# Performance work log

Hardware: AMD Instinct MI355X
Metric: run time of the kernel (lower is better)

Reference implementation:

```python
import math
import jax, jax.numpy as jnp
import numpy as np

VOCAB = 32000
D = 512
H = 4
N_LAYER = 4
B = 4
S = 512


def _ln(z, g, eps=1e-5):
    m = jnp.mean(z, axis=-1, keepdims=True)
    v = jnp.var(z, axis=-1, keepdims=True)
    return (z - m) * jax.lax.rsqrt(v + eps) * g


def setup_inputs() -> dict:
    key = jax.random.key(0)
    ks = jax.random.split(key, 6)
    std = 0.02
    x = jax.random.randint(ks[0], (B, S), 0, VOCAB)
    wte = jax.random.normal(ks[1], (VOCAB, D), jnp.float32) * std
    wpe = jax.random.normal(ks[2], (S + 1, D), jnp.float32) * std
    W_q = jax.random.normal(ks[3], (H, D, D), jnp.float32) * std
    W_k = jax.random.normal(ks[4], (H, D, D), jnp.float32) * std
    W_o = jax.random.normal(ks[5], (D, H * D), jnp.float32) * (std / math.sqrt(2 * N_LAYER))
    return {
        "x": x, "wte": wte, "wpe": wpe,
        "g_e": jnp.ones((D,), jnp.float32),
        "g_p": jnp.ones((D,), jnp.float32),
        "g_f": jnp.ones((D,), jnp.float32),
        "W_q": W_q, "W_k": W_k, "W_o": W_o,
    }


def reference(x, wte, wpe, g_e, g_p, g_f, W_q, W_k, W_o):
    b, s = x.shape
    d = wte.shape[1]

    # token / position embeddings (dropout p=0 -> identity)
    e = _ln(wte[x], g_e)                      # (B,S,D)
    p = _ln(wpe[: s + 1], g_p)                # (S+1,D), identical across batch
    x_i, x_j = p[:-1], p[1:]                  # keys / queries

    # custom QK attention kernel (batch-independent since p is shared)
    Q = jnp.einsum('sd,hde->hse', x_j, W_q)   # (H,S,D)
    K = jnp.einsum('sd,hde->hse', x_i, W_k)
    krn = jnp.einsum('hse,hte->hst', Q, K) / math.sqrt(d)
    krn = jnp.clip(krn, -10.0, 10.0)
    causal = jnp.tril(jnp.ones((s, s), bool))
    krn = jnp.where(causal, krn, -jnp.inf)
    krn = jax.nn.softmax(krn, axis=-1)        # (H,S,S)

    # W_N: row i scaled by 1/(i+1)
    coef = 1.0 / (1.0 + jnp.arange(s, dtype=e.dtype))  # (S,)

    f_k = jnp.zeros_like(e)
    for _ in range(N_LAYER):
        # soft codebook retrieval against full vocab
        scores = jnp.einsum('vd,bsd->bvs', wte, f_k)     # (B,V,S)
        R = jax.nn.softmax(scores, axis=-1)
        Rsum = jnp.sum(R, axis=1)                        # (B,S)
        ex_wte = jnp.einsum('bvs,vd->bsd', R, wte) / Rsum[..., None]
        Vm = e - ex_wte                                  # (B,S,D)
        delta = jnp.einsum('hst,btd->bhsd', krn, Vm)     # (B,H,S,D)
        delta = delta * coef[None, None, :, None]
        delta = delta.transpose(0, 2, 1, 3).reshape(b, s, -1)  # (B,S,H*D)
        f_k = f_k + delta @ W_o.T

    out = _ln(f_k, g_f)
    logits = out[:, -1:, :] @ wte.T                      # (B,1,V)
    return logits
```

## Files before the change

### kernel.cpp

```cpp
#include <hip/hip_runtime.h>
#include <stdint.h>


typedef __attribute__((ext_vector_type(8))) short s16x8;
typedef __attribute__((ext_vector_type(4))) short s16x4;
typedef __attribute__((ext_vector_type(4))) float f32x4;

__device__ __forceinline__ short f2bf(float f) {
  unsigned u = __float_as_uint(f);
  unsigned r = (u + 0x7FFFu + ((u >> 16) & 1u)) >> 16;
  return (short)r;
}
__device__ __forceinline__ float bf2f(short u) {
  unsigned v = ((unsigned)(unsigned short)u) << 16;
  return __uint_as_float(v);
}
__device__ __forceinline__ unsigned char f2fp8_full(float x) {
  unsigned u = __float_as_uint(x);
  unsigned sg = (u >> 24) & 0x80;
  u &= 0x7fffffff;
  float a = __uint_as_float(u);
  if (a >= 448.f) return (unsigned char)(sg | 0x7e);
  if (a < 0.015625f) {
    int m = (int)rintf(a * 512.f);
    return (unsigned char)(sg | m);
  }
  u += 0x7FFFFu + ((u >> 20) & 1u);
  int eb = (int)((u >> 23) & 0xff) - 120;
  if (eb >= 16) return (unsigned char)(sg | 0x7e);
  return (unsigned char)(sg | (eb << 3) | ((u >> 20) & 7));
}

__device__ __forceinline__ void load16(const void* g, void* l) {
  __builtin_amdgcn_global_load_lds(
      (__attribute__((address_space(1))) void*)g,
      (__attribute__((address_space(3))) void*)l, 16, 0, 0);
}

template <int EPI, int TERMS>
__global__ void __launch_bounds__(256) gemm64(
    const short* __restrict__ Ag, const short* __restrict__ Bg,
    const short* __restrict__ A2g, const short* __restrict__ B2g,
    void* __restrict__ Cg, short* __restrict__ C2g, int lda, int ldb, int ldc,
    int klen, int k0_mul, int zdiv, long sAq, long sAr, long sBq, long sBr,
    long sCq, long sCr) {
  const int tid = threadIdx.x;
  const int z = blockIdx.z;
  const int zq = z / zdiv, zr = z % zdiv;
  const long aOff = zq * sAq + zr * sAr + (long)zr * k0_mul;
  const long bOff = zq * sBq + zr * sBr + (long)zr * k0_mul;
  const long cOff = zq * sCq + zr * sCr;

  __shared__ __align__(16) short As[64 * 64];
  __shared__ __align__(16) short Bs[64 * 64];

  const long m0 = (long)blockIdx.x * 64;
  const long n0 = (long)blockIdx.y * 64;

  const int wave = tid >> 6, lane = tid & 63;
  const int wm = (wave >> 1) * 32, wn = (wave & 1) * 32;
  const int mlan = lane & 15, kg = lane >> 4;

  f32x4 acc[2][2] = {};

  const int g_src = ((lane & 7) ^ (lane >> 3)) * 8;
  const int lrow = lane >> 3;
  short* lA = As + wave * 1024 + lane * 8;
  short* lB = Bs + wave * 1024 + lane * 8;

  const int gi0 = ((kg ^ (mlan & 7)) * 8);
  const int gi1 = gi0 ^ 32;

  const int nk = klen >> 6;
#pragma unroll 1
  for (int t = 0; t < TERMS; ++t) {
    const short* Abase = ((TERMS == 3 && t == 2) ? A2g : Ag) + aOff;
    const short* Bbase = ((TERMS == 3 && t == 1) ? B2g : Bg) + bOff;
    const short* ga = Abase + (m0 + wave * 16 + lrow) * (long)lda + g_src;
    const short* gb = Bbase + (n0 + wave * 16 + lrow) * (long)ldb + g_src;
#pragma unroll 1
    for (int kt = 0; kt < nk; ++kt) {
      const int kb = kt * 64;
      __syncthreads();
      load16(ga + kb, lA);
      load16(ga + 8 * (long)lda + kb, lA + 512);
      load16(gb + kb, lB);
      load16(gb + 8 * (long)ldb + kb, lB + 512);
      __syncthreads();
      s16x8 af[2][2], bq[2][2];
      const short* pA = As + (wm + mlan) * 64;
      const short* pB = Bs + (wn + mlan) * 64;
#pragma unroll
      for (int i = 0; i < 2; ++i) {
        af[0][i] = *(const s16x8*)(pA + i * 1024 + gi0);
        af[1][i] = *(const s16x8*)(pA + i * 1024 + gi1);
        bq[0][i] = *(const s16x8*)(pB + i * 1024 + gi0);
        bq[1][i] = *(const s16x8*)(pB + i * 1024 + gi1);
      }
#pragma unroll
      for (int h = 0; h < 2; ++h)
#pragma unroll
        for (int mi = 0; mi < 2; ++mi)
#pragma unroll
          for (int ni = 0; ni < 2; ++ni)
            acc[mi][ni] = __builtin_amdgcn_mfma_f32_16x16x32_bf16(
                af[h][mi], bq[h][ni], acc[mi][ni], 0, 0, 0);
    }
  }

  const int rq = (lane >> 4) * 4;
#pragma unroll
  for (int mi = 0; mi < 2; ++mi) {
#pragma unroll
    for (int ni = 0; ni < 2; ++ni) {
#pragma unroll
      for (int r = 0; r < 4; ++r) {
        long row = m0 + wm + mi * 16 + rq + r;
        long col = n0 + wn + ni * 16 + mlan;
        float v = acc[mi][ni][r];
        long o = cOff + row * (long)ldc + col;
        if (EPI == 3) {
          ((float*)Cg)[o] = v;
        } else if (EPI == 4) {
          short h = f2bf(v);
          ((short*)Cg)[o] = h;
          C2g[o] = f2bf(v - bf2f(h));
        } else {
          ((short*)Cg)[o] = f2bf(v);
        }
      }
    }
  }
}

__global__ void __launch_bounds__(256) gemm8tri(
    const unsigned char* __restrict__ Ag, short* __restrict__ Cg) {
  const int tid = threadIdx.x;
  const int zr = blockIdx.z;
  const long kOff = (long)zr * 640;
  const long cOff = (long)zr * 262144;

  __shared__ __align__(16) unsigned char As[128 * 128];
  __shared__ __align__(16) unsigned char Bs[128 * 128];

  int t = blockIdx.x;
  int ty = 0;
  while ((ty + 1) * (ty + 2) / 2 <= t) ++ty;
  int tx = t - ty * (ty + 1) / 2;
  const long m0 = (long)tx * 128;
  const long n0 = (long)ty * 128;

  const int wave = tid >> 6, lane = tid & 63;
  const int wm = (wave >> 1) * 64, wn = (wave & 1) * 64;
  const int mlan = lane & 15, kg = lane >> 4;

  f32x4 acc[4][4] = {};

  const int g_src = ((lane & 7) ^ (lane >> 3)) * 16;
  const int lrow = lane >> 3;
  unsigned char* lA = As + wave * 4096 + lane * 16;
  unsigned char* lB = Bs + wave * 4096 + lane * 16;

  const unsigned char* ga = Ag + kOff + (m0 + wave * 32 + lrow) * 32000L + g_src;
  const unsigned char* gb = Ag + kOff + (n0 + wave * 32 + lrow) * 32000L + g_src;

#pragma unroll 1
  for (int kt = 0; kt < 5; ++kt) {
    const int kb = kt * 128;
    __syncthreads();
    load16(ga + kb, lA);
    load16(ga + 8 * 32000L + kb, lA + 1024);
    load16(ga + 16 * 32000L + kb, lA + 2048);
    load16(ga + 24 * 32000L + kb, lA + 3072);
    load16(gb + kb, lB);
    load16(gb + 8 * 32000L + kb, lB + 1024);
    load16(gb + 16 * 32000L + kb, lB + 2048);
    load16(gb + 24 * 32000L + kb, lB + 3072);
    __syncthreads();
    const unsigned char* pA = As + (wm + mlan) * 128;
    const unsigned char* pB = Bs + (wn + mlan) * 128;
#pragma unroll
    for (int h = 0; h < 4; ++h) {
      const int go = (((2 * h + (kg >> 1)) ^ (mlan & 7)) * 16) + (kg & 1) * 8;
      long af[4], bq[4];
#pragma unroll
      for (int i = 0; i < 4; ++i) {
        af[i] = *(const long*)(pA + i * 2048 + go);
        bq[i] = *(const long*)(pB + i * 2048 + go);
      }
#pragma unroll
      for (int mi = 0; mi < 4; ++mi)
#pragma unroll
        for (int ni = 0; ni < 4; ++ni)
          acc[mi][ni] = __builtin_amdgcn_mfma_f32_16x16x32_fp8_fp8(
              af[mi], bq[ni], acc[mi][ni], 0, 0, 0);
    }
  }

  const int rq = (lane >> 4) * 4;
#pragma unroll
  for (int mi = 0; mi < 4; ++mi)
#pragma unroll
    for (int ni = 0; ni < 4; ++ni)
#pragma unroll
      for (int r = 0; r < 4; ++r) {
        long row = m0 + wm + mi * 16 + rq + r;
        long col = n0 + wn + ni * 16 + mlan;
        Cg[cOff + row * 512 + col] = f2bf(acc[mi][ni][r]);
      }
}

__global__ void __launch_bounds__(256) ln_both(
    const int* __restrict__ tok, const float* __restrict__ wte,
    const float* __restrict__ wpe, const float* __restrict__ g_e,
    const float* __restrict__ g_p, float* __restrict__ e32,
    short* __restrict__ p_hi, short* __restrict__ p_lo) {
  int r = blockIdx.x, tid = threadIdx.x;
  bool tokm = r < 2048;
  const float* in =
      tokm ? wte + (long)tok[r] * 512 : wpe + (long)(r - 2048) * 512;
  const float* g = tokm ? g_e : g_p;
  int d = tid * 2;
  float2 v = *(const float2*)(in + d);
  float s1 = v.x + v.y;
  float s2 = v.x * v.x + v.y * v.y;
  __shared__ float red[20];
  for (int o = 32; o > 0; o >>= 1) {
    s1 += __shfl_down(s1, o);
    s2 += __shfl_down(s2, o);
  }
  int wave = tid >> 6, lane = tid & 63;
  if (lane == 0) { red[wave] = s1; red[wave + 8] = s2; }
  __syncthreads();
  if (tid == 0) {
    float a = red[0] + red[1] + red[2] + red[3];
    float b = red[8] + red[9] + red[10] + red[11];
    float mean = a * (1.f / 512.f);
    float var = b * (1.f / 512.f) - mean * mean;
    red[16] = mean;
    red[17] = 1.0f / sqrtf(var + 1e-5f);
  }
  __syncthreads();
  float mean = red[16], rs = red[17];
  float2 gg = *(const float2*)(g + d);
  float y0 = (v.x - mean) * rs * gg.x;
  float y1 = (v.y - mean) * rs * gg.y;
  if (tokm) {
    long o = (long)r * 512 + d;
    e32[o] = y0;
    e32[o + 1] = y1;
  } else {
    long o = (long)(r - 2048) * 512 + d;
    short h0 = f2bf(y0), h1 = f2bf(y1);
    p_hi[o] = h0; p_hi[o + 1] = h1;
    p_lo[o] = f2bf(y0 - bf2f(h0));
    p_lo[o + 1] = f2bf(y1 - bf2f(h1));
  }
}

__global__ void __launch_bounds__(256) softmax_krn_k(
    const float* __restrict__ raw, float* __restrict__ klast,
    short* __restrict__ k16) {
  int bx = blockIdx.x;
  int h = bx >> 9, s = bx & 511;
  long base = ((long)h * 512 + s) * 512;
  int tid = threadIdx.x;
  const float scale = 0.04419417382415922f;
  float e0 = 0.f, e1 = 0.f, l = 0.f;
  int t0 = tid, t1 = tid + 256;
  if (t0 <= s) {
    float v = raw[base + t0] * scale;
    v = fminf(fmaxf(v, -10.f), 10.f);
    e0 = __expf(v); l += e0;
  }
  if (t1 <= s) {
    float v = raw[base + t1] * scale;
    v = fminf(fmaxf(v, -10.f), 10.f);
    e1 = __expf(v); l += e1;
  }
  for (int o = 32; o > 0; o >>= 1) l += __shfl_down(l, o);
  __shared__ float red[10];
  int wave = tid >> 6, lane = tid & 63;
  if (lane == 0) red[wave] = l;
  __syncthreads();
  if (tid == 0) red[8] = 1.0f / (red[0] + red[1] + red[2] + red[3]);
  __syncthreads();
  float inv = red[8];
  float coef = 1.0f / (1.0f + (float)s);
  k16[base + t0] = f2bf(e0 * inv * coef);
  k16[base + t1] = f2bf(e1 * inv * coef);
  if (s == 511) {
    klast[h * 512 + t0] = e0 * inv;
    klast[h * 512 + t1] = e1 * inv;
  }
}

__global__ void __launch_bounds__(256) prep_w(
    const float* __restrict__ Wq, const float* __restrict__ Wk,
    const float* __restrict__ W_o, short* __restrict__ hi,
    short* __restrict__ lo, short* __restrict__ wo16,
    float* __restrict__ WoT) {
  int z = blockIdx.z;
  int tid = threadIdx.x;
  __shared__ float tl[64][65];
  if (z < 8) {
    const float* inp =
        (z < 4) ? Wq + (long)z * 262144 : Wk + (long)(z - 4) * 262144;
    short* ho = hi + (long)z * 262144;
    short* lop = lo + (long)z * 262144;
    int c0 = blockIdx.x * 64, r0 = blockIdx.y * 64;
    for (int it = 0; it < 16; ++it) {
      int idx = it * 256 + tid;
      int rr = idx >> 6, cc = idx & 63;
      tl[rr][cc] = inp[(long)(r0 + rr) * 512 + (c0 + cc)];
    }
    __syncthreads();
    for (int it = 0; it < 16; ++it) {
      int idx = it * 256 + tid;
      int rr = idx >> 6, cc = idx & 63;
      float v = tl[cc][rr];
      long o = (long)(c0 + rr) * 512 + (r0 + cc);
      short hh = f2bf(v);
      ho[o] = hh;
      lop[o] = f2bf(v - bf2f(hh));
    }
  } else {
    int c0 = (blockIdx.x + (z - 8) * 8) * 64, r0 = blockIdx.y * 64;
    for (int it = 0; it < 16; ++it) {
      int idx = it * 256 + tid;
      int rr = idx >> 6, cc = idx & 63;
      long o = (long)(r0 + rr) * 2048 + (c0 + cc);
      float v = W_o[o];
      tl[rr][cc] = v;
      wo16[o] = f2bf(v);
    }
    __syncthreads();
    for (int it = 0; it < 16; ++it) {
      int idx = it * 256 + tid;
      int rr = idx >> 6, cc = idx & 63;
      WoT[(long)(c0 + rr) * 512 + (r0 + cc)] = tl[cc][rr];
    }
  }
}

__global__ void __launch_bounds__(256) prep_wte(
    const float* __restrict__ wte, unsigned char* __restrict__ wT8,
    float* __restrict__ cm) {
  int c0 = blockIdx.x * 64, r0 = blockIdx.y * 64;
  __shared__ float tl[64][65];
  __shared__ float cred[4][64];
  int tid = threadIdx.x, w = tid >> 6, cx = tid & 63;
  float csum = 0.f;
  for (int it = 0; it < 16; ++it) {
    int idx = it * 256 + tid;
    int rr = idx >> 6, cc = idx & 63;
    float v = wte[(long)(r0 + rr) * 512 + c0 + cc];
    tl[rr][cc] = v;
    csum += v;
  }
  cred[w][cx] = csum;
  __syncthreads();
  if (w == 0) {
    float s = cred[0][cx] + cred[1][cx] + cred[2][cx] + cred[3][cx];
    atomicAdd(&cm[c0 + cx], s * (1.f / 32000.f));
  }
  for (int it = 0; it < 16; ++it) {
    int idx = it * 256 + tid;
    int rr = idx >> 6, cc = idx & 63;
    wT8[(long)(c0 + rr) * 32000 + r0 + cc] = f2fp8_full(tl[cc][rr] * 64.f);
  }
}

__global__ void __launch_bounds__(256) gsum_k(
    const short* __restrict__ part, short* __restrict__ G16) {
  int t = blockIdx.x;
  int ty = 0;
  while ((ty + 1) * (ty + 2) / 2 <= t) ++ty;
  int tx = t - ty * (ty + 1) / 2;
  int r0 = blockIdx.y * 16;
  int tid = threadIdx.x;
  float acc[8] = {};
  for (int z = 0; z < 50; ++z) {
    const short* p = part + (long)z * 262144;
#pragma unroll
    for (int it = 0; it < 8; ++it) {
      int idx = it * 256 + tid;
      int r = idx >> 7, c = idx & 127;
      acc[it] += bf2f(p[(long)(tx * 128 + r0 + r) * 512 + ty * 128 + c]);
    }
  }
  __shared__ short tl[16][132];
#pragma unroll
  for (int it = 0; it < 8; ++it) {
    int idx = it * 256 + tid;
    int r = idx >> 7, c = idx & 127;
    short h = f2bf(acc[it] * (1.f / 4096.f));
    G16[(long)(tx * 128 + r0 + r) * 512 + ty * 128 + c] = h;
    tl[r][c] = h;
  }
  if (tx == ty) return;
  __syncthreads();
#pragma unroll
  for (int it = 0; it < 8; ++it) {
    int idx = it * 256 + tid;
    int c = idx >> 4, r = idx & 15;
    G16[(long)(ty * 128 + c) * 512 + tx * 128 + r0 + r] = tl[r][c];
  }
}

__global__ void __launch_bounds__(256) gmean_k(
    const short* __restrict__ gc, const float* __restrict__ rowdot,
    float* __restrict__ fbarG, float* __restrict__ fbcm,
    float* __restrict__ dl) {
  int b = blockIdx.y, e0 = blockIdx.x * 64;
  int tid = threadIdx.x, w = tid >> 6, lane = tid & 63;
  dl[(long)(b * 8 + blockIdx.x) * 256 + tid] = 0.f;
  float acc = 0.f;
  const short* p = gc + (long)b * 262144 + e0 + lane;
  for (int s = w * 128; s < w * 128 + 128; ++s) acc += bf2f(p[(long)s * 512]);
  __shared__ float red[4][64];
  red[w][lane] = acc;
  __syncthreads();
  if (w == 0)
    fbarG[b * 512 + e0 + lane] =
        (red[0][lane] + red[1][lane] + red[2][lane] + red[3][lane]) *
        (1.f / 512.f);
  if (blockIdx.x == 0) {
    float r2 = rowdot[b * 512 + tid] + rowdot[b * 512 + 256 + tid];
    for (int o = 32; o > 0; o >>= 1) r2 += __shfl_down(r2, o);
    __shared__ float rr[4];
    if (lane == 0) rr[w] = r2;
    __syncthreads();
    if (tid == 0) fbcm[b] = (rr[0] + rr[1] + rr[2] + rr[3]) * (1.f / 512.f);
  }
}

__global__ void __launch_bounds__(256) vm_k(
    const float* __restrict__ e32, const short* __restrict__ gc,
    const float* __restrict__ cm, const float* __restrict__ fbarG,
    const float* __restrict__ rowdot, const float* __restrict__ fbcm,
    const float* __restrict__ klast, int useCm, int store,
    short* __restrict__ vmT, float* __restrict__ dl) {
  int b = blockIdx.z, t0 = blockIdx.y * 64, e0 = blockIdx.x * 64;
  __shared__ short tl[64][72];
  __shared__ float kl[4][64];
  __shared__ float ri[64];
  __shared__ float cmv[64];
  __shared__ float fbg[64];
  __shared__ float dred[4][4][64];
  int tid = threadIdx.x;
  int w = tid >> 6, cx = tid & 63;
  kl[w][cx] = klast[w * 512 + t0 + cx];
  if (tid < 64)
    ri[tid] =
        useCm ? 1.f : 1.0f / (1.0f + rowdot[b * 512 + t0 + tid] - fbcm[b]);
  if (tid >= 64 && tid < 128) cmv[tid - 64] = cm[e0 + tid - 64];
  if (tid >= 128 && tid < 192)
    fbg[tid - 128] = useCm ? 0.f : fbarG[b * 512 + e0 + tid - 128];
  __syncthreads();
  long base = ((long)b * 512 + t0) * 512 + e0;
  float accH[4] = {0.f, 0.f, 0.f, 0.f};
  for (int it = 0; it < 16; ++it) {
    int idx = it * 256 + tid;
    int rr = idx >> 6, cc = idx & 63;
    long o = base + (long)rr * 512 + cc;
    float ex;
    if (useCm)
      ex = cmv[cc];
    else
      ex = (cmv[cc] + (bf2f(gc[o]) - fbg[cc]) * (1.f / 32000.f)) * ri[rr];
    float v = e32[o] - ex;
    if (store) tl[rr][cc] = f2bf(v);
#pragma unroll
    for (int h = 0; h < 4; ++h) accH[h] += v * kl[h][rr];
  }
#pragma unroll
  for (int h = 0; h < 4; ++h) dred[w][h][cx] = accH[h];
  __syncthreads();
  if (store) {
    for (int it = 0; it < 16; ++it) {
      int idx = it * 256 + tid;
      int rr = idx >> 6, cc = idx & 63;
      vmT[((long)b * 512 + (e0 + rr)) * 512 + (t0 + cc)] = tl[cc][rr];
    }
  }
  float s = dred[0][w][cx] + dred[1][w][cx] + dred[2][w][cx] + dred[3][w][cx];
  atomicAdd(&dl[(long)b * 2048 + w * 512 + e0 + cx], s * (1.f / 512.f));
}

__global__ void __launch_bounds__(256) flast_k(
    const float* __restrict__ dl, const float* __restrict__ WoT,
    float* __restrict__ fl, float* __restrict__ rowdot) {
  int b = blockIdx.y, d0 = blockIdx.x * 64;
  int tid = threadIdx.x, w = tid >> 6, lane = tid & 63;
  int g = (blockIdx.y * 8 + blockIdx.x) * 256 + tid;
  if (g < 2048) rowdot[g] = 0.f;
  __shared__ float ds[2048];
  __shared__ float red[4][64];
  for (int i = tid; i < 2048; i += 256) ds[i] = dl[(long)b * 2048 + i];
  __syncthreads();
  float acc = 0.f;
  const float* wp = WoT + (long)(w * 512) * 512 + d0 + lane;
  for (int k = 0; k < 512; ++k) acc += ds[w * 512 + k] * wp[(long)k * 512];
  red[w][lane] = acc;
  __syncthreads();
  if (w == 0) {
    float s = red[0][lane] + red[1][lane] + red[2][lane] + red[3][lane];
    fl[(long)b * 512 + d0 + lane] += s;
  }
}

__global__ void __launch_bounds__(256) fkupdate_k(
    const short* __restrict__ part, const float* __restrict__ cm,
    float* __restrict__ fk32, short* __restrict__ fk16,
    float* __restrict__ rowdot) {
  long i = (long)blockIdx.x * 256 + threadIdx.x;
  float4 s = ((const float4*)fk32)[i];
#pragma unroll
  for (int p = 0; p < 4; ++p) {
    s16x4 h = *(const s16x4*)(part + (long)p * 1048576 + i * 4);
    s.x += bf2f(h[0]); s.y += bf2f(h[1]);
    s.z += bf2f(h[2]); s.w += bf2f(h[3]);
  }
  ((float4*)fk32)[i] = s;
  s16x4 o;
  o[0] = f2bf(s.x); o[1] = f2bf(s.y); o[2] = f2bf(s.z); o[3] = f2bf(s.w);
  *(s16x4*)(fk16 + i * 4) = o;
  float4 cmv = ((const float4*)cm)[i & 127];
  float d = s.x * cmv.x + s.y * cmv.y + s.z * cmv.z + s.w * cmv.w;
  for (int off = 32; off > 0; off >>= 1) d += __shfl_down(d, off);
  if ((threadIdx.x & 63) == 0) atomicAdd(&rowdot[i >> 7], d);
}

__global__ void __launch_bounds__(256) logits_k(
    const float* __restrict__ flast, const float* __restrict__ g_f,
    const float* __restrict__ wte, float* __restrict__ out) {
  int tid = threadIdx.x, wave = tid >> 6, lane = tid & 63;
  __shared__ float oln[4][512];
  __shared__ float red[20];
  for (int b = 0; b < 4; ++b) {
    int d = tid * 2;
    float2 v = *(const float2*)(flast + b * 512 + d);
    float s1 = v.x + v.y;
    float s2 = v.x * v.x + v.y * v.y;
    for (int o = 32; o > 0; o >>= 1) {
      s1 += __shfl_down(s1, o);
      s2 += __shfl_down(s2, o);
    }
    if (lane == 0) { red[wave] = s1; red[wave + 8] = s2; }
    __syncthreads();
    if (tid == 0) {
      float a = red[0] + red[1] + red[2] + red[3];
      float bb = red[8] + red[9] + red[10] + red[11];
      float mean = a * (1.f / 512.f);
      float var = bb * (1.f / 512.f) - mean * mean;
      red[16] = mean;
      red[17] = 1.0f / sqrtf(var + 1e-5f);
    }
    __syncthreads();
    float mean = red[16], rs = red[17];
    float2 gg = *(const float2*)(g_f + d);
    oln[b][d] = (v.x - mean) * rs * gg.x;
    oln[b][d + 1] = (v.y - mean) * rs * gg.y;
    __syncthreads();
  }
  float o[4][8];
#pragma unroll
  for (int b = 0; b < 4; b++)
#pragma unroll
    for (int j = 0; j < 8; j++) o[b][j] = oln[b][lane * 8 + j];
  int vbase = blockIdx.x * 64 + wave * 16;
  for (int i = 0; i < 16; i++) {
    int v = vbase + i;
    const float* row = wte + (long)v * 512 + lane * 8;
    float4 x0 = *(const float4*)row;
    float4 x1 = *(const float4*)(row + 4);
    float xr[8] = {x0.x, x0.y, x0.z, x0.w, x1.x, x1.y, x1.z, x1.w};
    float d0 = 0, d1 = 0, d2 = 0, d3 = 0;
#pragma unroll
    for (int j = 0; j < 8; j++) {
      d0 += o[0][j] * xr[j]; d1 += o[1][j] * xr[j];
      d2 += o[2][j] * xr[j]; d3 += o[3][j] * xr[j];
    }
    for (int off = 32; off > 0; off >>= 1) {
      d0 += __shfl_down(d0, off); d1 += __shfl_down(d1, off);
      d2 += __shfl_down(d2, off); d3 += __shfl_down(d3, off);
    }
    if (lane == 0) {
      out[v] = d0; out[32000 + v] = d1; out[64000 + v] = d2;
      out[96000 + v] = d3;
    }
  }
}

extern "C" void kernel_launch(void* const* d_in, const int* in_sizes, int n_in,
                              void* d_out, int out_size, void* d_ws,
                              size_t ws_size, hipStream_t stream) {
  (void)in_sizes; (void)n_in; (void)out_size;
  const int* x = (const int*)d_in[0];
  const float* wte = (const float*)d_in[1];
  const float* wpe = (const float*)d_in[2];
  const float* g_e = (const float*)d_in[3];
  const float* g_p = (const float*)d_in[4];
  const float* g_f = (const float*)d_in[5];
  const float* W_q = (const float*)d_in[6];
  const float* W_k = (const float*)d_in[7];
  const float* W_o = (const float*)d_in[8];
  float* out = (float*)d_out;

  char* ws = (char*)d_ws;
  size_t off = 0;
  auto alloc = [&](size_t b) {
    size_t o = off;
    off += (b + 255) & ~(size_t)255;
    return o;
  };
  const long HS = 262144;
  unsigned char* wT8 = (unsigned char*)(ws + alloc(512L * 32000));
  char* u = ws + alloc(10L * 1048576 * 2);
  short* wqkt_hi = (short*)u;
  short* wqkt_lo = (short*)(u + 4194304);
  short* qk_hi = (short*)(u + 8388608);
  short* qk_lo = (short*)(u + 12582912);
  float* sATT = (float*)(u + 16777216);
  short* fkpart = (short*)u;
  short* wo16 = (short*)(ws + alloc(512L * 2048 * 2));
  float* WoT = (float*)(ws + alloc(2048L * 512 * 4));
  short* p_hi = (short*)(ws + alloc(513L * 512 * 2));
  short* p_lo = (short*)(ws + alloc(513L * 512 * 2));
  float* e32 = (float*)(ws + alloc(2048L * 512 * 4));
  size_t zero_off = off;
  float* colmean = (float*)(ws + alloc(512 * 4));
  float* dl = (float*)(ws + alloc(4L * 2048 * 4));
  float* flast = (float*)(ws + alloc(4L * 512 * 4));
  float* fk32 = (float*)(ws + alloc(2048L * 512 * 4));
  size_t zero_len = off - zero_off;
  float* klast = (float*)(ws + alloc(4L * 512 * 4));
  short* krn16 = (short*)(ws + alloc(4L * HS * 2));
  short* Gpart16 = (short*)(ws + alloc(50L * HS * 2));
  short* G16 = (short*)(ws + alloc(512L * 512 * 2));
  short* fk16b = (short*)(ws + alloc(2048L * 512 * 2));
  short* gc16 = (short*)(ws + alloc(2048L * 512 * 2));
  float* fbarG = (float*)(ws + alloc(4L * 512 * 4));
  float* rowdot = (float*)(ws + alloc(2052L * 4));
  float* fbcm = rowdot + 2048;
  short* vmT16 = (short*)(ws + alloc(2048L * 512 * 2));
  short* delta16 = (short*)(ws + alloc(2048L * 2048 * 2));
  if (off > ws_size) return;

  hipMemsetAsync(ws + zero_off, 0, zero_len, stream);

  prep_wte<<<dim3(8, 500), 256, 0, stream>>>(wte, wT8, colmean);
  gemm8tri<<<dim3(10, 1, 50), 256, 0, stream>>>(wT8, Gpart16);
  gsum_k<<<dim3(10, 8), 256, 0, stream>>>(Gpart16, G16);
  prep_w<<<dim3(8, 8, 12), 256, 0, stream>>>(W_q, W_k, W_o, wqkt_hi, wqkt_lo,
                                             wo16, WoT);
  ln_both<<<2561, 256, 0, stream>>>(x, wte, wpe, g_e, g_p, e32, p_hi, p_lo);

  gemm64<4, 3><<<dim3(8, 8, 8), 256, 0, stream>>>(
      p_hi + 512, wqkt_hi, p_lo + 512, wqkt_lo, qk_hi, qk_lo, 512, 512, 512,
      512, 0, 4,  -512,  0,  4 * HS,  HS,
       4 * HS,  HS);
  gemm64<3, 3><<<dim3(8, 8, 4), 256, 0, stream>>>(
      qk_hi, qk_hi + 4 * HS, qk_lo, qk_lo + 4 * HS, sATT, nullptr, 512, 512,
      512, 512, 0, 4, 0, HS, 0, HS, 0, HS);
  softmax_krn_k<<<2048, 256, 0, stream>>>(sATT, klast, krn16);

  for (int l = 0; l < 4; ++l) {
    if (l > 0) {
      gemm64<0, 1><<<dim3(32, 8, 1), 256, 0, stream>>>(
          fk16b, G16, nullptr, nullptr, gc16, nullptr, 512, 512, 512, 512, 0,
          1, 0, 0, 0, 0, 0, 0);
      gmean_k<<<dim3(8, 4), 256, 0, stream>>>(gc16, rowdot, fbarG, fbcm, dl);
    }
    vm_k<<<dim3(8, 8, 4), 256, 0, stream>>>(
        e32, gc16, colmean, fbarG, rowdot, fbcm, klast, (l == 0) ? 1 : 0,
        (l < 3) ? 1 : 0, vmT16, dl);
    flast_k<<<dim3(8, 4), 256, 0, stream>>>(dl, WoT, flast, rowdot);
    if (l < 3) {
      gemm64<0, 1><<<dim3(8, 8, 16), 256, 0, stream>>>(
          krn16, vmT16, nullptr, nullptr, delta16, nullptr, 512, 512, 2048,
          512, 0, 4, 0, HS, HS, 0, 1048576L, 512);
      gemm64<0, 1><<<dim3(32, 8, 4), 256, 0, stream>>>(
          delta16, wo16, nullptr, nullptr, fkpart, nullptr, 2048, 2048, 512,
          512, 512, 4, 0, 0, 0, 0, 0, 1048576L);
      fkupdate_k<<<1024, 256, 0, stream>>>(fkpart, colmean, fk32, fk16b,
                                           rowdot);
    }
  }

  logits_k<<<500, 256, 0, stream>>>(flast, g_f, wte, out);
}
```

Measured before the change: 445.1 us.

## Merge independent setup and per-layer kernels into horizontally fused launches

Independent kernels are combined into single launches that dispatch on block index: the weight prep and layernorm kernels become one setup kernel, the fp8 Gram GEMM shares a launch with the QK projection GEMM, the Gram reduction shares one with the attention-score GEMM, and flast shares one with the delta GEMM. The goal is to cut launch overhead and idle tails on small grids by letting independent work overlap. In exchange, every block of a fused kernel reserves the larger shared-memory allocation, which may lower occupancy, and branching by block index can leave the work unevenly balanced.

```diff
diff --git a/kernel.cpp b/kernel.cpp
--- a/kernel.cpp
+++ b/kernel.cpp
@@ -38,24 +38,22 @@
 }
 
 template <int EPI, int TERMS>
-__global__ void __launch_bounds__(256) gemm64(
-    const short* __restrict__ Ag, const short* __restrict__ Bg,
-    const short* __restrict__ A2g, const short* __restrict__ B2g,
-    void* __restrict__ Cg, short* __restrict__ C2g, int lda, int ldb, int ldc,
-    int klen, int k0_mul, int zdiv, long sAq, long sAr, long sBq, long sBr,
-    long sCq, long sCr) {
+__device__ __forceinline__ void gemm64_body(
+    char* smem, int bx, int by, int bz, const short* Ag, const short* Bg,
+    const short* A2g, const short* B2g, void* Cg, short* C2g, int lda,
+    int ldb, int ldc, int klen, int k0_mul, int zdiv, long sAq, long sAr,
+    long sBq, long sBr, long sCq, long sCr) {
   const int tid = threadIdx.x;
-  const int z = blockIdx.z;
-  const int zq = z / zdiv, zr = z % zdiv;
+  const int zq = bz / zdiv, zr = bz % zdiv;
   const long aOff = zq * sAq + zr * sAr + (long)zr * k0_mul;
   const long bOff = zq * sBq + zr * sBr + (long)zr * k0_mul;
   const long cOff = zq * sCq + zr * sCr;
 
-  __shared__ __align__(16) short As[64 * 64];
-  __shared__ __align__(16) short Bs[64 * 64];
-
-  const long m0 = (long)blockIdx.x * 64;
-  const long n0 = (long)blockIdx.y * 64;
+  short* As = (short*)smem;
+  short* Bs = (short*)(smem + 8192);
+
+  const long m0 = (long)bx * 64;
+  const long n0 = (long)by * 64;
 
   const int wave = tid >> 6, lane = tid & 63;
   const int wm = (wave >> 1) * 32, wn = (wave & 1) * 32;
@@ -133,17 +131,30 @@
   }
 }
 
-__global__ void __launch_bounds__(256) gemm8tri(
-    const unsigned char* __restrict__ Ag, short* __restrict__ Cg) {
+template <int EPI, int TERMS>
+__global__ void __launch_bounds__(256) gemm64(
+    const short* __restrict__ Ag, const short* __restrict__ Bg,
+    const short* __restrict__ A2g, const short* __restrict__ B2g,
+    void* __restrict__ Cg, short* __restrict__ C2g, int lda, int ldb, int ldc,
+    int klen, int k0_mul, int zdiv, long sAq, long sAr, long sBq, long sBr,
+    long sCq, long sCr) {
+  __shared__ __align__(16) char smem[16384];
+  gemm64_body<EPI, TERMS>(smem, blockIdx.x, blockIdx.y, blockIdx.z, Ag, Bg,
+                          A2g, B2g, Cg, C2g, lda, ldb, ldc, klen, k0_mul,
+                          zdiv, sAq, sAr, sBq, sBr, sCq, sCr);
+}
+
+__device__ __forceinline__ void gemm8tri_body(char* smem, int bxx, int bzz,
+                                              const unsigned char* Ag,
+                                              short* Cg) {
   const int tid = threadIdx.x;
-  const int zr = blockIdx.z;
-  const long kOff = (long)zr * 640;
-  const long cOff = (long)zr * 262144;
-
-  __shared__ __align__(16) unsigned char As[128 * 128];
-  __shared__ __align__(16) unsigned char Bs[128 * 128];
-
-  int t = blockIdx.x;
+  const long kOff = (long)bzz * 640;
+  const long cOff = (long)bzz * 262144;
+
+  unsigned char* As = (unsigned char*)smem;
+  unsigned char* Bs = (unsigned char*)(smem + 16384);
+
+  int t = bxx;
   int ty = 0;
   while ((ty + 1) * (ty + 2) / 2 <= t) ++ty;
   int tx = t - ty * (ty + 1) / 2;
@@ -161,8 +172,10 @@
   unsigned char* lA = As + wave * 4096 + lane * 16;
   unsigned char* lB = Bs + wave * 4096 + lane * 16;
 
-  const unsigned char* ga = Ag + kOff + (m0 + wave * 32 + lrow) * 32000L + g_src;
-  const unsigned char* gb = Ag + kOff + (n0 + wave * 32 + lrow) * 32000L + g_src;
+  const unsigned char* ga =
+      Ag + kOff + (m0 + wave * 32 + lrow) * 32000L + g_src;
+  const unsigned char* gb =
+      Ag + kOff + (n0 + wave * 32 + lrow) * 32000L + g_src;
 
 #pragma unroll 1
   for (int kt = 0; kt < 5; ++kt) {
@@ -210,51 +223,244 @@
       }
 }
 
-__global__ void __launch_bounds__(256) ln_both(
-    const int* __restrict__ tok, const float* __restrict__ wte,
+__device__ __forceinline__ void gsum_body(char* smem, int bxx, int byy,
+                                          const short* part, short* G16) {
+  int t = bxx;
+  int ty = 0;
+  while ((ty + 1) * (ty + 2) / 2 <= t) ++ty;
+  int tx = t - ty * (ty + 1) / 2;
+  int r0 = byy * 16;
+  int tid = threadIdx.x;
+  short* tl = (short*)smem;
+  float acc[8] = {};
+  for (int z = 0; z < 50; ++z) {
+    const short* p = part + (long)z * 262144;
+#pragma unroll
+    for (int it = 0; it < 8; ++it) {
+      int idx = it * 256 + tid;
+      int r = idx >> 7, c = idx & 127;
+      acc[it] += bf2f(p[(long)(tx * 128 + r0 + r) * 512 + ty * 128 + c]);
+    }
+  }
+#pragma unroll
+  for (int it = 0; it < 8; ++it) {
+    int idx = it * 256 + tid;
+    int r = idx >> 7, c = idx & 127;
+    short h = f2bf(acc[it] * (1.f / 4096.f));
+    G16[(long)(tx * 128 + r0 + r) * 512 + ty * 128 + c] = h;
+    tl[r * 132 + c] = h;
+  }
+  if (tx == ty) return;
+  __syncthreads();
+#pragma unroll
+  for (int it = 0; it < 8; ++it) {
+    int idx = it * 256 + tid;
+    int c = idx >> 4, r = idx & 15;
+    G16[(long)(ty * 128 + c) * 512 + tx * 128 + r0 + r] = tl[r * 132 + c];
+  }
+}
+
+__device__ __forceinline__ void flast_body(char* smem, int bxx, int byy,
+                                           const float* dl, const float* WoT,
+                                           float* fl, float* rowdot) {
+  int b = byy, d0 = bxx * 64;
+  int tid = threadIdx.x, w = tid >> 6, lane = tid & 63;
+  float* ds = (float*)smem;
+  float* red = (float*)(smem + 8192);
+  int g = (byy * 8 + bxx) * 256 + tid;
+  if (g < 2048) rowdot[g] = 0.f;
+  for (int i = tid; i < 2048; i += 256) ds[i] = dl[(long)b * 2048 + i];
+  __syncthreads();
+  float acc = 0.f;
+  const float* wp = WoT + (long)(w * 512) * 512 + d0 + lane;
+  for (int k = 0; k < 512; ++k) acc += ds[w * 512 + k] * wp[(long)k * 512];
+  red[w * 64 + lane] = acc;
+  __syncthreads();
+  if (w == 0) {
+    float s = red[lane] + red[64 + lane] + red[128 + lane] + red[192 + lane];
+    fl[(long)b * 512 + d0 + lane] += s;
+  }
+}
+
+__global__ void __launch_bounds__(256) triqk_k(
+    const unsigned char* __restrict__ wT8, short* __restrict__ Gpart16,
+    const short* __restrict__ p_hi, const short* __restrict__ wqkt_hi,
+    const short* __restrict__ p_lo, const short* __restrict__ wqkt_lo,
+    short* __restrict__ qk_hi, short* __restrict__ qk_lo) {
+  __shared__ __align__(16) char smem[32768];
+  const long HS = 262144;
+  int b = blockIdx.x;
+  if (b < 500) {
+    gemm8tri_body(smem, b % 10, b / 10, wT8, Gpart16);
+  } else {
+    int q = b - 500;
+    gemm64_body<4, 3>(smem, q & 7, (q >> 3) & 7, q >> 6, p_hi, wqkt_hi, p_lo,
+                      wqkt_lo, qk_hi, qk_lo, 512, 512, 512, 512, 0, 4,
+                       -512,  0,  4 * HS,  HS,
+                       4 * HS,  HS);
+  }
+}
+
+__global__ void __launch_bounds__(256) gsumqkt_k(
+    const short* __restrict__ Gpart16, short* __restrict__ G16,
+    const short* __restrict__ qk_hi, const short* __restrict__ qk_lo,
+    float* __restrict__ sATT) {
+  __shared__ __align__(16) char smem[16384];
+  const long HS = 262144;
+  int b = blockIdx.x;
+  if (b < 256) {
+    gemm64_body<3, 3>(smem, b & 7, (b >> 3) & 7, b >> 6, qk_hi, qk_hi + 4 * HS,
+                      qk_lo, qk_lo + 4 * HS, sATT, nullptr, 512, 512, 512,
+                      512, 0, 4, 0, HS, 0, HS, 0, HS);
+  } else {
+    int t = b - 256;
+    gsum_body(smem, t % 10, t / 10, Gpart16, G16);
+  }
+}
+
+__global__ void __launch_bounds__(256) flastdelta_k(
+    const short* __restrict__ krn16, const short* __restrict__ vmT16,
+    short* __restrict__ delta16, const float* __restrict__ dl,
+    const float* __restrict__ WoT, float* __restrict__ fl,
+    float* __restrict__ rowdot) {
+  __shared__ __align__(16) char smem[16384];
+  const long HS = 262144;
+  int b = blockIdx.x;
+  if (b < 1024) {
+    gemm64_body<0, 1>(smem, b & 7, (b >> 3) & 7, b >> 6, krn16, vmT16,
+                      nullptr, nullptr, delta16, nullptr, 512, 512, 2048, 512,
+                      0, 4, 0, HS, HS, 0, 1048576L, 512);
+  } else {
+    int t = b - 1024;
+    flast_body(smem, t & 7, t >> 3, dl, WoT, fl, rowdot);
+  }
+}
+
+__global__ void __launch_bounds__(256) flast_k(
+    const float* __restrict__ dl, const float* __restrict__ WoT,
+    float* __restrict__ fl, float* __restrict__ rowdot) {
+  __shared__ __align__(16) char smem[9216];
+  flast_body(smem, blockIdx.x, blockIdx.y, dl, WoT, fl, rowdot);
+}
+
+__global__ void __launch_bounds__(256) setup_all(
+    const float* __restrict__ wte, unsigned char* __restrict__ wT8,
+    float* __restrict__ cm, const float* __restrict__ Wq,
+    const float* __restrict__ Wk, const float* __restrict__ W_o,
+    short* __restrict__ hi, short* __restrict__ lo, short* __restrict__ wo16,
+    float* __restrict__ WoT, const int* __restrict__ tok,
     const float* __restrict__ wpe, const float* __restrict__ g_e,
     const float* __restrict__ g_p, float* __restrict__ e32,
     short* __restrict__ p_hi, short* __restrict__ p_lo) {
-  int r = blockIdx.x, tid = threadIdx.x;
-  bool tokm = r < 2048;
-  const float* in =
-      tokm ? wte + (long)tok[r] * 512 : wpe + (long)(r - 2048) * 512;
-  const float* g = tokm ? g_e : g_p;
-  int d = tid * 2;
-  float2 v = *(const float2*)(in + d);
-  float s1 = v.x + v.y;
-  float s2 = v.x * v.x + v.y * v.y;
+  __shared__ float tl[64][65];
+  __shared__ float cred[4][64];
   __shared__ float red[20];
-  for (int o = 32; o > 0; o >>= 1) {
-    s1 += __shfl_down(s1, o);
-    s2 += __shfl_down(s2, o);
-  }
-  int wave = tid >> 6, lane = tid & 63;
-  if (lane == 0) { red[wave] = s1; red[wave + 8] = s2; }
-  __syncthreads();
-  if (tid == 0) {
-    float a = red[0] + red[1] + red[2] + red[3];
-    float b = red[8] + red[9] + red[10] + red[11];
-    float mean = a * (1.f / 512.f);
-    float var = b * (1.f / 512.f) - mean * mean;
-    red[16] = mean;
-    red[17] = 1.0f / sqrtf(var + 1e-5f);
-  }
-  __syncthreads();
-  float mean = red[16], rs = red[17];
-  float2 gg = *(const float2*)(g + d);
-  float y0 = (v.x - mean) * rs * gg.x;
-  float y1 = (v.y - mean) * rs * gg.y;
-  if (tokm) {
-    long o = (long)r * 512 + d;
-    e32[o] = y0;
-    e32[o + 1] = y1;
+  int blk = blockIdx.x;
+  int tid = threadIdx.x;
+  if (blk < 4000) {
+    int c0 = (blk & 7) * 64, r0 = (blk >> 3) * 64;
+    int w = tid >> 6, cx = tid & 63;
+    float csum = 0.f;
+    for (int it = 0; it < 16; ++it) {
+      int idx = it * 256 + tid;
+      int rr = idx >> 6, cc = idx & 63;
+      float v = wte[(long)(r0 + rr) * 512 + c0 + cc];
+      tl[rr][cc] = v;
+      csum += v;
+    }
+    cred[w][cx] = csum;
+    __syncthreads();
+    if (w == 0) {
+      float s = cred[0][cx] + cred[1][cx] + cred[2][cx] + cred[3][cx];
+      atomicAdd(&cm[c0 + cx], s * (1.f / 32000.f));
+    }
+    for (int it = 0; it < 16; ++it) {
+      int idx = it * 256 + tid;
+      int rr = idx >> 6, cc = idx & 63;
+      wT8[(long)(c0 + rr) * 32000 + r0 + cc] = f2fp8_full(tl[cc][rr] * 64.f);
+    }
+  } else if (blk < 4768) {
+    int t = blk - 4000;
+    int z = t >> 6, by = (t >> 3) & 7, bx = t & 7;
+    if (z < 8) {
+      const float* inp =
+          (z < 4) ? Wq + (long)z * 262144 : Wk + (long)(z - 4) * 262144;
+      short* ho = hi + (long)z * 262144;
+      short* lop = lo + (long)z * 262144;
+      int c0 = bx * 64, r0 = by * 64;
+      for (int it = 0; it < 16; ++it) {
+        int idx = it * 256 + tid;
+        int rr = idx >> 6, cc = idx & 63;
+        tl[rr][cc] = inp[(long)(r0 + rr) * 512 + (c0 + cc)];
+      }
+      __syncthreads();
+      for (int it = 0; it < 16; ++it) {
+        int idx = it * 256 + tid;
+        int rr = idx >> 6, cc = idx & 63;
+        float v = tl[cc][rr];
+        long o = (long)(c0 + rr) * 512 + (r0 + cc);
+        short hh = f2bf(v);
+        ho[o] = hh;
+        lop[o] = f2bf(v - bf2f(hh));
+      }
+    } else {
+      int c0 = (bx + (z - 8) * 8) * 64, r0 = by * 64;
+      for (int it = 0; it < 16; ++it) {
+        int idx = it * 256 + tid;
+        int rr = idx >> 6, cc = idx & 63;
+        long o = (long)(r0 + rr) * 2048 + (c0 + cc);
+        float v = W_o[o];
+        tl[rr][cc] = v;
+        wo16[o] = f2bf(v);
+      }
+      __syncthreads();
+      for (int it = 0; it < 16; ++it) {
+        int idx = it * 256 + tid;
+        int rr = idx >> 6, cc = idx & 63;
+        WoT[(long)(c0 + rr) * 512 + (r0 + cc)] = tl[cc][rr];
+      }
+    }
   } else {
-    long o = (long)(r - 2048) * 512 + d;
-    short h0 = f2bf(y0), h1 = f2bf(y1);
-    p_hi[o] = h0; p_hi[o + 1] = h1;
-    p_lo[o] = f2bf(y0 - bf2f(h0));
-    p_lo[o + 1] = f2bf(y1 - bf2f(h1));
+    int r = blk - 4768;
+    bool tokm = r < 2048;
+    const float* in =
+        tokm ? wte + (long)tok[r] * 512 : wpe + (long)(r - 2048) * 512;
+    const float* g = tokm ? g_e : g_p;
+    int d = tid * 2;
+    float2 v = *(const float2*)(in + d);
+    float s1 = v.x + v.y;
+    float s2 = v.x * v.x + v.y * v.y;
+    for (int o = 32; o > 0; o >>= 1) {
+      s1 += __shfl_down(s1, o);
+      s2 += __shfl_down(s2, o);
+    }
+    int wave = tid >> 6, lane = tid & 63;
+    if (lane == 0) { red[wave] = s1; red[wave + 8] = s2; }
+    __syncthreads();
+    if (tid == 0) {
+      float a = red[0] + red[1] + red[2] + red[3];
+      float b2 = red[8] + red[9] + red[10] + red[11];
+      float mean = a * (1.f / 512.f);
+      float var = b2 * (1.f / 512.f) - mean * mean;
+      red[16] = mean;
+      red[17] = 1.0f / sqrtf(var + 1e-5f);
+    }
+    __syncthreads();
+    float mean = red[16], rs = red[17];
+    float2 gg = *(const float2*)(g + d);
+    float y0 = (v.x - mean) * rs * gg.x;
+    float y1 = (v.y - mean) * rs * gg.y;
+    if (tokm) {
+      long o = (long)r * 512 + d;
+      e32[o] = y0;
+      e32[o + 1] = y1;
+    } else {
+      long o = (long)(r - 2048) * 512 + d;
+      short h0 = f2bf(y0), h1 = f2bf(y1);
+      p_hi[o] = h0; p_hi[o + 1] = h1;
+      p_lo[o] = f2bf(y0 - bf2f(h0));
+      p_lo[o + 1] = f2bf(y1 - bf2f(h1));
+    }
   }
 }
 
@@ -292,119 +498,6 @@
   if (s == 511) {
     klast[h * 512 + t0] = e0 * inv;
     klast[h * 512 + t1] = e1 * inv;
-  }
-}
-
-__global__ void __launch_bounds__(256) prep_w(
-    const float* __restrict__ Wq, const float* __restrict__ Wk,
-    const float* __restrict__ W_o, short* __restrict__ hi,
-    short* __restrict__ lo, short* __restrict__ wo16,
-    float* __restrict__ WoT) {
-  int z = blockIdx.z;
-  int tid = threadIdx.x;
-  __shared__ float tl[64][65];
-  if (z < 8) {
-    const float* inp =
-        (z < 4) ? Wq + (long)z * 262144 : Wk + (long)(z - 4) * 262144;
-    short* ho = hi + (long)z * 262144;
-    short* lop = lo + (long)z * 262144;
-    int c0 = blockIdx.x * 64, r0 = blockIdx.y * 64;
-    for (int it = 0; it < 16; ++it) {
-      int idx = it * 256 + tid;
-      int rr = idx >> 6, cc = idx & 63;
-      tl[rr][cc] = inp[(long)(r0 + rr) * 512 + (c0 + cc)];
-    }
-    __syncthreads();
-    for (int it = 0; it < 16; ++it) {
-      int idx = it * 256 + tid;
-      int rr = idx >> 6, cc = idx & 63;
-      float v = tl[cc][rr];
-      long o = (long)(c0 + rr) * 512 + (r0 + cc);
-      short hh = f2bf(v);
-      ho[o] = hh;
-      lop[o] = f2bf(v - bf2f(hh));
-    }
-  } else {
-    int c0 = (blockIdx.x + (z - 8) * 8) * 64, r0 = blockIdx.y * 64;
-    for (int it = 0; it < 16; ++it) {
-      int idx = it * 256 + tid;
-      int rr = idx >> 6, cc = idx & 63;
-      long o = (long)(r0 + rr) * 2048 + (c0 + cc);
-      float v = W_o[o];
-      tl[rr][cc] = v;
-      wo16[o] = f2bf(v);
-    }
-    __syncthreads();
-    for (int it = 0; it < 16; ++it) {
-      int idx = it * 256 + tid;
-      int rr = idx >> 6, cc = idx & 63;
-      WoT[(long)(c0 + rr) * 512 + (r0 + cc)] = tl[cc][rr];
-    }
-  }
-}
-
-__global__ void __launch_bounds__(256) prep_wte(
-    const float* __restrict__ wte, unsigned char* __restrict__ wT8,
-    float* __restrict__ cm) {
-  int c0 = blockIdx.x * 64, r0 = blockIdx.y * 64;
-  __shared__ float tl[64][65];
-  __shared__ float cred[4][64];
-  int tid = threadIdx.x, w = tid >> 6, cx = tid & 63;
-  float csum = 0.f;
-  for (int it = 0; it < 16; ++it) {
-    int idx = it * 256 + tid;
-    int rr = idx >> 6, cc = idx & 63;
-    float v = wte[(long)(r0 + rr) * 512 + c0 + cc];
-    tl[rr][cc] = v;
-    csum += v;
-  }
-  cred[w][cx] = csum;
-  __syncthreads();
-  if (w == 0) {
-    float s = cred[0][cx] + cred[1][cx] + cred[2][cx] + cred[3][cx];
-    atomicAdd(&cm[c0 + cx], s * (1.f / 32000.f));
-  }
-  for (int it = 0; it < 16; ++it) {
-    int idx = it * 256 + tid;
-    int rr = idx >> 6, cc = idx & 63;
-    wT8[(long)(c0 + rr) * 32000 + r0 + cc] = f2fp8_full(tl[cc][rr] * 64.f);
-  }
-}
-
-__global__ void __launch_bounds__(256) gsum_k(
-    const short* __restrict__ part, short* __restrict__ G16) {
-  int t = blockIdx.x;
-  int ty = 0;
-  while ((ty + 1) * (ty + 2) / 2 <= t) ++ty;
-  int tx = t - ty * (ty + 1) / 2;
-  int r0 = blockIdx.y * 16;
-  int tid = threadIdx.x;
-  float acc[8] = {};
-  for (int z = 0; z < 50; ++z) {
-    const short* p = part + (long)z * 262144;
-#pragma unroll
-    for (int it = 0; it < 8; ++it) {
-      int idx = it * 256 + tid;
-      int r = idx >> 7, c = idx & 127;
-      acc[it] += bf2f(p[(long)(tx * 128 + r0 + r) * 512 + ty * 128 + c]);
-    }
-  }
-  __shared__ short tl[16][132];
-#pragma unroll
-  for (int it = 0; it < 8; ++it) {
-    int idx = it * 256 + tid;
-    int r = idx >> 7, c = idx & 127;
-    short h = f2bf(acc[it] * (1.f / 4096.f));
-    G16[(long)(tx * 128 + r0 + r) * 512 + ty * 128 + c] = h;
-    tl[r][c] = h;
-  }
-  if (tx == ty) return;
-  __syncthreads();
-#pragma unroll
-  for (int it = 0; it < 8; ++it) {
-    int idx = it * 256 + tid;
-    int c = idx >> 4, r = idx & 15;
-    G16[(long)(ty * 128 + c) * 512 + tx * 128 + r0 + r] = tl[r][c];
   }
 }
 
@@ -486,28 +579,6 @@
   }
   float s = dred[0][w][cx] + dred[1][w][cx] + dred[2][w][cx] + dred[3][w][cx];
   atomicAdd(&dl[(long)b * 2048 + w * 512 + e0 + cx], s * (1.f / 512.f));
-}
-
-__global__ void __launch_bounds__(256) flast_k(
-    const float* __restrict__ dl, const float* __restrict__ WoT,
-    float* __restrict__ fl, float* __restrict__ rowdot) {
-  int b = blockIdx.y, d0 = blockIdx.x * 64;
-  int tid = threadIdx.x, w = tid >> 6, lane = tid & 63;
-  int g = (blockIdx.y * 8 + blockIdx.x) * 256 + tid;
-  if (g < 2048) rowdot[g] = 0.f;
-  __shared__ float ds[2048];
-  __shared__ float red[4][64];
-  for (int i = tid; i < 2048; i += 256) ds[i] = dl[(long)b * 2048 + i];
-  __syncthreads();
-  float acc = 0.f;
-  const float* wp = WoT + (long)(w * 512) * 512 + d0 + lane;
-  for (int k = 0; k < 512; ++k) acc += ds[w * 512 + k] * wp[(long)k * 512];
-  red[w][lane] = acc;
-  __syncthreads();
-  if (w == 0) {
-    float s = red[0][lane] + red[1][lane] + red[2][lane] + red[3][lane];
-    fl[(long)b * 512 + d0 + lane] += s;
-  }
 }
 
 __global__ void __launch_bounds__(256) fkupdate_k(
@@ -650,20 +721,12 @@
 
   hipMemsetAsync(ws + zero_off, 0, zero_len, stream);
 
-  prep_wte<<<dim3(8, 500), 256, 0, stream>>>(wte, wT8, colmean);
-  gemm8tri<<<dim3(10, 1, 50), 256, 0, stream>>>(wT8, Gpart16);
-  gsum_k<<<dim3(10, 8), 256, 0, stream>>>(Gpart16, G16);
-  prep_w<<<dim3(8, 8, 12), 256, 0, stream>>>(W_q, W_k, W_o, wqkt_hi, wqkt_lo,
-                                             wo16, WoT);
-  ln_both<<<2561, 256, 0, stream>>>(x, wte, wpe, g_e, g_p, e32, p_hi, p_lo);
-
-  gemm64<4, 3><<<dim3(8, 8, 8), 256, 0, stream>>>(
-      p_hi + 512, wqkt_hi, p_lo + 512, wqkt_lo, qk_hi, qk_lo, 512, 512, 512,
-      512, 0, 4,  -512,  0,  4 * HS,  HS,
-       4 * HS,  HS);
-  gemm64<3, 3><<<dim3(8, 8, 4), 256, 0, stream>>>(
-      qk_hi, qk_hi + 4 * HS, qk_lo, qk_lo + 4 * HS, sATT, nullptr, 512, 512,
-      512, 512, 0, 4, 0, HS, 0, HS, 0, HS);
+  setup_all<<<7329, 256, 0, stream>>>(wte, wT8, colmean, W_q, W_k, W_o,
+                                      wqkt_hi, wqkt_lo, wo16, WoT, x, wpe,
+                                      g_e, g_p, e32, p_hi, p_lo);
+  triqk_k<<<1012, 256, 0, stream>>>(wT8, Gpart16, p_hi + 512, wqkt_hi,
+                                    p_lo + 512, wqkt_lo, qk_hi, qk_lo);
+  gsumqkt_k<<<336, 256, 0, stream>>>(Gpart16, G16, qk_hi, qk_lo, sATT);
   softmax_krn_k<<<2048, 256, 0, stream>>>(sATT, klast, krn16);
 
   for (int l = 0; l < 4; ++l) {
@@ -676,16 +739,16 @@
     vm_k<<<dim3(8, 8, 4), 256, 0, stream>>>(
         e32, gc16, colmean, fbarG, rowdot, fbcm, klast, (l == 0) ? 1 : 0,
         (l < 3) ? 1 : 0, vmT16, dl);
-    flast_k<<<dim3(8, 4), 256, 0, stream>>>(dl, WoT, flast, rowdot);
     if (l < 3) {
-      gemm64<0, 1><<<dim3(8, 8, 16), 256, 0, stream>>>(
-          krn16, vmT16, nullptr, nullptr, delta16, nullptr, 512, 512, 2048,
-          512, 0, 4, 0, HS, HS, 0, 1048576L, 512);
+      flastdelta_k<<<1056, 256, 0, stream>>>(krn16, vmT16, delta16, dl, WoT,
+                                             flast, rowdot);
       gemm64<0, 1><<<dim3(32, 8, 4), 256, 0, stream>>>(
           delta16, wo16, nullptr, nullptr, fkpart, nullptr, 2048, 2048, 512,
           512, 512, 4, 0, 0, 0, 0, 0, 1048576L);
       fkupdate_k<<<1024, 256, 0, stream>>>(fkpart, colmean, fk32, fk16b,
                                            rowdot);
+    } else {
+      flast_k<<<dim3(8, 4), 256, 0, stream>>>(dl, WoT, flast, rowdot);
     }
   }
 
```

Measured after the change: 404.6 us. 9.1% less time.
